# Kernel tuning notes

Measured on AMD Instinct MI355X. Metric: run time of the kernel, lower is better.

The kernel has to match this reference:

```python
import jax, jax.numpy as jnp
import numpy as np

EPS = 1e-8
EPS12 = 1e-12
TAU = 0.2
IOU_THRESHOLD = 0.5
NEG_INF = -1e9

N, C = 8192, 1024
HID, FGD, CLSD = 256, 64, 128


def setup_inputs() -> dict:
    key = jax.random.key(0)
    ks = jax.random.split(key, 16)
    roi_feats = jax.random.normal(ks[0], (N, C), dtype=jnp.float32)
    # labels in {-1 (ignore), 0 (bg), 1..20 (classes)}
    labels = jax.random.randint(ks[1], (N,), 0, 21, dtype=jnp.int64) - 1
    ious = jax.random.uniform(ks[2], (N,), dtype=jnp.float32)
    s = 0.02
    w1f = jax.random.normal(ks[3], (HID, C), dtype=jnp.float32) * s
    b1f = jnp.zeros((HID,), dtype=jnp.float32)
    w2f = jax.random.normal(ks[4], (FGD, HID), dtype=jnp.float32) * s
    b2f = jnp.zeros((FGD,), dtype=jnp.float32)
    w1c = jax.random.normal(ks[5], (HID, C), dtype=jnp.float32) * s
    b1c = jnp.zeros((HID,), dtype=jnp.float32)
    w2c = jax.random.normal(ks[6], (CLSD, HID), dtype=jnp.float32) * s
    b2c = jnp.zeros((CLSD,), dtype=jnp.float32)
    return {"roi_feats": roi_feats, "labels": labels, "ious": ious,
            "w1f": w1f, "b1f": b1f, "w2f": w2f, "b2f": b2f,
            "w1c": w1c, "b1c": b1c, "w2c": w2c, "b2c": b2c}


def _project_normalize(x, w1, b1, w2, b2):
    h = jax.nn.relu(x @ w1.T + b1)
    z = h @ w2.T + b2
    nrm = jnp.linalg.norm(z, axis=1, keepdims=True)  # F.normalize: z / max(||z||, eps)
    return z / jnp.maximum(nrm, EPS)


def _fg_bg_loss(z_fg, fg_mask, ignore_mask, iou_weight):
    n = z_fg.shape[0]
    anchor = fg_mask & ~ignore_mask
    eye = jnp.eye(n, dtype=bool)
    # pos_mask[i,j] = fg_mask[j] & ~ignore[j], self excluded
    pos = (fg_mask & ~ignore_mask)[None, :] & ~eye  # [N,N]
    sim = (z_fg @ z_fg.T) / TAU
    sim_exp = jnp.exp(sim) * (~eye).astype(sim.dtype)
    denom = sim_exp.sum(axis=1)  # [N]
    numer = jnp.sum(jnp.exp(sim) * pos.astype(sim.dtype), axis=1)  # [N]
    n_pos = pos.sum(axis=1)
    loss_i = -jnp.log((numer + EPS) / (denom + EPS))
    valid = anchor & (n_pos > 0)
    w = iou_weight
    num = jnp.sum(jnp.where(valid, loss_i * w, 0.0))
    den = jnp.sum(jnp.where(valid, w, 0.0)) + EPS
    return num / den


def _class_supcon_loss(z_cls, labels, fg_mask, ignore_mask, iou_weight):
    n = z_cls.shape[0]
    anchor = fg_mask & ~ignore_mask
    eye = jnp.eye(n, dtype=bool)
    valid_den = ~eye & ~ignore_mask[None, :]  # [N,N]
    # pos[i,j]: same label, j not ignored, labels[j] != 0, j != i, j valid
    pos = (labels[None, :] == labels[:, None]) & ~ignore_mask[None, :] & (labels[None, :] != 0)
    pos = pos & ~eye & valid_den
    sim = (z_cls @ z_cls.T) / TAU
    logits = jnp.where(valid_den, sim, NEG_INF)
    denom_log = jax.nn.logsumexp(logits, axis=1)  # [N]
    n_pos = pos.sum(axis=1)
    sum_pos = jnp.sum(jnp.where(pos, sim, 0.0), axis=1)
    n_pos_safe = jnp.maximum(n_pos, 1).astype(sim.dtype)
    loss_i = -(sum_pos - n_pos.astype(sim.dtype) * denom_log) / n_pos_safe
    valid = anchor & (n_pos > 0) & valid_den.any(axis=1)
    w = iou_weight
    num = jnp.sum(jnp.where(valid, loss_i * w, 0.0))
    den = jnp.sum(jnp.where(valid, w, 0.0)) + EPS12
    return num / den


def reference(roi_feats, labels, ious, w1f, b1f, w2f, b2f, w1c, b1c, w2c, b2c):
    z_fg = _project_normalize(roi_feats, w1f, b1f, w2f, b2f)
    z_cls = _project_normalize(roi_feats, w1c, b1c, w2c, b2c)
    ignore_mask = labels == -1
    bg_mask = (labels == 0) & ~ignore_mask
    fg_mask = (labels > 0) & ~ignore_mask
    iou_weight = jnp.where(ious > IOU_THRESHOLD, ious, 0.0)
    loss_fg_bg = _fg_bg_loss(z_fg, fg_mask, ignore_mask, iou_weight)
    loss_supcon = _class_supcon_loss(z_cls, labels, fg_mask, ignore_mask, iou_weight)
    # loss_weights = (1.0, 1.0); stacked as [loss_fg_bg, loss_supcon]
    return jnp.stack([loss_fg_bg * 1.0, loss_supcon * 1.0])
```

## Files before the change

### kernel.cpp

```cpp
#include <hip/hip_runtime.h>
#include <hip/hip_bf16.h>
#include <math.h>

#define N_ROI 8192
#define C_IN  1024
#define HIDD  256
#define FGD   64
#define CLSD  128
#define INV_TAU 5.0f
#define SCALE_LOG2E 7.2134752f
#define LN2F 0.69314718f

using frag_ab = __attribute__((ext_vector_type(8))) short;
using f32x16  = __attribute__((ext_vector_type(16))) float;

static __device__ __forceinline__ short f32_to_bf16_bits(float f) {
  unsigned u = __builtin_bit_cast(unsigned, f);
  u = (u + 0x7FFFu + ((u >> 16) & 1u)) >> 16;
  return (short)u;
}
static __device__ __forceinline__ float bf16_bits_to_f32(short b) {
  unsigned u = ((unsigned)(unsigned short)b) << 16;
  return __builtin_bit_cast(float, u);
}
static __device__ __forceinline__ float fast_exp2(float x) {
#if __has_builtin(__builtin_amdgcn_exp2f)
  return __builtin_amdgcn_exp2f(x);
#else
  return exp2f(x);
#endif
}
static __device__ __forceinline__ void async_copy16(const void* g, void* l) {
  __builtin_amdgcn_global_load_lds(
      (const __attribute__((address_space(1))) unsigned int*)g,
      (__attribute__((address_space(3))) unsigned int*)l, 16, 0, 0);
}

__global__ __launch_bounds__(256) void pack_zero_kernel(
    const float* __restrict__ X,
    const float* __restrict__ w1f, const float* __restrict__ w1c,
    const float* __restrict__ w2f, const float* __restrict__ w2c,
    short* __restrict__ W1pf, short* __restrict__ W1pc,
    short* __restrict__ W2pf, short* __restrict__ W2pc,
    short* __restrict__ Xp16,
    float* __restrict__ accum, int* __restrict__ cnt,
    float* __restrict__ Vc) {
  int b = blockIdx.x;
  if (b == 280) {
    int t = threadIdx.x;
    if (t < 8) accum[t] = 0.f;
    if (t < 24) cnt[t] = 0;
    for (int q = t; q < 2560; q += 256) Vc[q] = 0.f;
    return;
  }
  if (b >= 281) {
    int b2 = b - 281;
    int Mb = b2 >> 4, cpair = b2 & 15;
    int tid = threadIdx.x;
    int c = cpair * 2 + (tid >> 7);
    int tt = tid & 127;
    int lane = tt & 63, kh = tt >> 6;
    int row = lane & 31, hi = lane >> 5;
    const float* src = X + (size_t)(Mb * 32 + row) * C_IN + c * 32 + kh * 16 + hi * 8;
    float4 v0 = *(const float4*)src;
    float4 v1 = *(const float4*)(src + 4);
    union { short s[8]; uint4 v; } o;
    o.s[0] = f32_to_bf16_bits(v0.x); o.s[1] = f32_to_bf16_bits(v0.y);
    o.s[2] = f32_to_bf16_bits(v0.z); o.s[3] = f32_to_bf16_bits(v0.w);
    o.s[4] = f32_to_bf16_bits(v1.x); o.s[5] = f32_to_bf16_bits(v1.y);
    o.s[6] = f32_to_bf16_bits(v1.z); o.s[7] = f32_to_bf16_bits(v1.w);
    *(uint4*)&Xp16[((size_t)(Mb * 32 + c)) * 1024 + (size_t)tt * 8] = o.v;
    return;
  }
  const float* src; short* dst; int Ksh; int b0;
  if (b < 128)      { src = w1f; dst = W1pf; Ksh = 10; b0 = 0; }
  else if (b < 256) { src = w1c; dst = W1pc; Ksh = 10; b0 = 128; }
  else if (b < 264) { src = w2f; dst = W2pf; Ksh = 8;  b0 = 256; }
  else              { src = w2c; dst = W2pc; Ksh = 8;  b0 = 264; }
  int K = 1 << Ksh;
  int f = (b - b0) * 256 + threadIdx.x;
  int r = f >> (Ksh - 3);
  int c0 = (f & ((K >> 3) - 1)) << 3;
  float4 v0 = *(const float4*)(src + (size_t)r * K + c0);
  float4 v1 = *(const float4*)(src + (size_t)r * K + c0 + 4);
  union { short s[8]; uint4 v; } o;
  o.s[0] = f32_to_bf16_bits(v0.x); o.s[1] = f32_to_bf16_bits(v0.y);
  o.s[2] = f32_to_bf16_bits(v0.z); o.s[3] = f32_to_bf16_bits(v0.w);
  o.s[4] = f32_to_bf16_bits(v1.x); o.s[5] = f32_to_bf16_bits(v1.y);
  o.s[6] = f32_to_bf16_bits(v1.z); o.s[7] = f32_to_bf16_bits(v1.w);
  ((uint4*)dst)[(size_t)((r >> 5) * (K >> 4) + (c0 >> 4)) * 64 +
                ((c0 >> 3) & 1) * 32 + (r & 31)] = o.v;
}

template<int D>
__device__ __forceinline__ void gemm2_from_lds(
    const short* __restrict__ T2,
    const short* __restrict__ W2p, const float* __restrict__ b2,
    short* __restrict__ Zr, float* __restrict__ tii,
    short* __restrict__ T, int gt) {
  int lane = threadIdx.x & 63;
  const frag_ab* Wv = (const frag_ab*)W2p;
  constexpr int NT = D / 32;
  frag_ab a[16];
  #pragma unroll
  for (int kc = 0; kc < 16; ++kc)
    a[kc] = *(const frag_ab*)&T2[(lane & 31) * 264 + kc * 16 + (lane >> 5) * 8];
  f32x16 acc[NT];
  #pragma unroll
  for (int j = 0; j < NT; ++j)
    #pragma unroll
    for (int q = 0; q < 16; ++q) acc[j][q] = 0.f;
  #pragma unroll
  for (int kc = 0; kc < 16; ++kc)
    #pragma unroll
    for (int j = 0; j < NT; ++j)
      acc[j] = __builtin_amdgcn_mfma_f32_32x32x16_bf16(a[kc], Wv[(j * 16 + kc) * 64 + lane], acc[j], 0, 0, 0);
  int c = lane & 31, h = lane >> 5;
  float bb[NT];
  #pragma unroll
  for (int j = 0; j < NT; ++j) bb[j] = b2[j * 32 + c];
  float s1[16];
  #pragma unroll
  for (int r = 0; r < 16; ++r) {
    s1[r] = 0.f;
    #pragma unroll
    for (int j = 0; j < NT; ++j) {
      float v = acc[j][r] + bb[j];
      s1[r] += v * v;
    }
  }
  #pragma unroll
  for (int r = 0; r < 16; ++r)
    #pragma unroll
    for (int m = 1; m < 32; m <<= 1) s1[r] += __shfl_xor(s1[r], m);
  float s2[16];
  #pragma unroll
  for (int r = 0; r < 16; ++r) s2[r] = 0.f;
  #pragma unroll
  for (int j = 0; j < NT; ++j) {
    int cl = j * 32 + c;
    #pragma unroll
    for (int g = 0; g < 4; ++g) {
      short q0, q1, q2, q3;
      #pragma unroll
      for (int e = 0; e < 4; ++e) {
        int r = g * 4 + e;
        float sc = 1.f / fmaxf(sqrtf(s1[r]), 1e-8f);
        short qb = f32_to_bf16_bits((acc[j][r] + bb[j]) * sc);
        float zf = bf16_bits_to_f32(qb);
        s2[r] += zf * zf;
        if (e == 0) q0 = qb; else if (e == 1) q1 = qb; else if (e == 2) q2 = qb; else q3 = qb;
      }
      *(short4*)&T[cl * 36 + 4 * h + 8 * g] = make_short4(q0, q1, q2, q3);
    }
  }
  #pragma unroll
  for (int r = 0; r < 16; ++r)
    #pragma unroll
    for (int m = 1; m < 32; m <<= 1) s2[r] += __shfl_xor(s2[r], m);
  if (c == 0) {
    #pragma unroll
    for (int r = 0; r < 16; ++r)
      tii[gt * 32 + (r & 3) + 8 * (r >> 2) + 4 * h] = s2[r];
  }
  uint4* Zv = (uint4*)Zr;
  #pragma unroll
  for (int k = 0; k < D / 16; ++k) {
    int c0 = (2 * k + h) * 8;
    union { short s[8]; uint4 u; } o;
    #pragma unroll
    for (int e = 0; e < 8; ++e) o.s[e] = T[(c0 + e) * 36 + c];
    Zv[(size_t)(gt * (D / 16) + k) * 64 + h * 32 + c] = o.u;
  }
}

__global__ __launch_bounds__(256) void fused_mlp_kernel(
    const short* __restrict__ Xp16,
    const short* __restrict__ W1pf, const short* __restrict__ W1pc,
    const float* __restrict__ b1f, const float* __restrict__ b1c,
    const short* __restrict__ W2pf, const short* __restrict__ W2pc,
    const float* __restrict__ b2f, const float* __restrict__ b2c,
    short* __restrict__ Zrf, short* __restrict__ Zrc,
    float* __restrict__ tiif, float* __restrict__ tiic,
    const int* __restrict__ labels,
    float* __restrict__ Sfg, float* __restrict__ Pfg,
    float* __restrict__ Scls,
    float* __restrict__ pfv, float* __restrict__ nimv,
    int* __restrict__ cnt) {
  __shared__ short ringA[4 * 1024];
  __shared__ short T2[32 * 264];
  __shared__ short Tw[128 * 36];
  int tid = threadIdx.x, lane = tid & 63, wv = tid >> 6;
  int Mb = blockIdx.x, head = blockIdx.y;

  if (head == 0 && tid < 32) {
    int i = Mb * 32 + tid;
    Sfg[i] = 0.f; Pfg[i] = 0.f; Scls[i] = 0.f;
    int l = labels[i];
    pfv[i]  = (l > 0)  ? 1.f : 0.f;
    nimv[i] = (l != -1) ? 1.f : 0.f;
    int b = l + 1; if (b < 0) b = 0; if (b > 21) b = 21;
    atomicAdd(&cnt[b], 1);
  }
  __builtin_amdgcn_sched_barrier(0);
  asm volatile("s_waitcnt vmcnt(0)" ::: "memory");
  __builtin_amdgcn_sched_barrier(0);

  const short* Wp = head ? W1pc : W1pf;
  const float* b1 = head ? b1c  : b1f;
  const uint4* Wv4 = (const uint4*)Wp;
  int t127 = tid & 127;

  frag_ab breg[3][4];
  f32x16 acc[2];
  #pragma unroll
  for (int nt = 0; nt < 2; ++nt)
    #pragma unroll
    for (int q = 0; q < 16; ++q) acc[nt][q] = 0.f;

  auto stageA = [&](int c, int slot) {
    const short* src = Xp16 + ((size_t)(Mb * 32 + c)) * 1024 + (size_t)t127 * 8;
    async_copy16(src, &ringA[slot * 1024 + t127 * 8]);
  };
  auto loadB = [&](int c, int s) {
    #pragma unroll
    for (int kci = 0; kci < 2; ++kci)
      #pragma unroll
      for (int nt = 0; nt < 2; ++nt)
        breg[s][kci * 2 + nt] =
            *(const frag_ab*)&Wv4[(size_t)((wv * 2 + nt) * 64 + c * 2 + kci) * 64 + lane];
  };
  auto domfma = [&](int slot, int bank) {
    frag_ab a0 = *(const frag_ab*)&ringA[slot * 1024 + (0 * 64 + lane) * 8];
    frag_ab a1 = *(const frag_ab*)&ringA[slot * 1024 + (1 * 64 + lane) * 8];
    #pragma unroll
    for (int nt = 0; nt < 2; ++nt)
      acc[nt] = __builtin_amdgcn_mfma_f32_32x32x16_bf16(a0, breg[bank][nt], acc[nt], 0, 0, 0);
    #pragma unroll
    for (int nt = 0; nt < 2; ++nt)
      acc[nt] = __builtin_amdgcn_mfma_f32_32x32x16_bf16(a1, breg[bank][2 + nt], acc[nt], 0, 0, 0);
  };

  stageA(0, 0); stageA(1, 1); loadB(0, 0); stageA(2, 2); loadB(1, 1);

  #pragma unroll
  for (int c = 0; c < 32; ++c) {
    if (c < 30)       asm volatile("s_waitcnt vmcnt(5)" ::: "memory");
    else if (c == 30) asm volatile("s_waitcnt vmcnt(4)" ::: "memory");
    else              asm volatile("s_waitcnt vmcnt(0)" ::: "memory");
    __builtin_amdgcn_s_barrier();
    __builtin_amdgcn_sched_barrier(0);
    if (c + 3 < 32) stageA(c + 3, (c + 3) & 3);
    if (c + 2 < 32) loadB(c + 2, (c + 2) % 3);
    domfma(c & 3, c % 3);
  }
  {
    int cl31 = lane & 31, h = lane >> 5;
    #pragma unroll
    for (int nt = 0; nt < 2; ++nt) {
      int gc = wv * 64 + nt * 32 + cl31;
      float bb = b1[gc];
      #pragma unroll
      for (int q = 0; q < 16; ++q) {
        int row = (q & 3) + 8 * (q >> 2) + 4 * h;
        float x = fmaxf(acc[nt][q] + bb, 0.f);
        T2[row * 264 + gc] = f32_to_bf16_bits(x);
      }
    }
  }
  __syncthreads();

  if (wv == 0) {
    if (head == 0)
      gemm2_from_lds<FGD>(T2, W2pf, b2f, Zrf, tiif, Tw, Mb);
    else
      gemm2_from_lds<CLSD>(T2, W2pc, b2c, Zrc, tiic, Tw, Mb);
  }
}

__global__ __launch_bounds__(128) void classsum_kernel(
    const short* __restrict__ Zrc, const int* __restrict__ labels,
    float* __restrict__ Vc) {
  __shared__ int lidx[512];
  __shared__ int lcnt;
  int c = blockIdx.x + 1;
  int d = threadIdx.x;
  int j0 = blockIdx.y * 512;
  if (d == 0) lcnt = 0;
  __syncthreads();
  #pragma unroll
  for (int u = 0; u < 4; ++u) {
    int row = j0 + u * 128 + d;
    if (labels[row] == c) {
      int k = atomicAdd(&lcnt, 1);
      lidx[k] = row;
    }
  }
  __syncthreads();
  int n = lcnt;
  int kc = d >> 4, h = (d >> 3) & 1, e = d & 7;
  float acc = 0.f;
  for (int k = 0; k < n; ++k) {
    int row = lidx[k];
    int jt = row >> 5, r = row & 31;
    acc += bf16_bits_to_f32(
        Zrc[((size_t)((jt * 8 + kc) * 64 + h * 32 + r)) * 8 + e]);
  }
  atomicAdd(&Vc[(c - 1) * 128 + d], acc);
}

template<int D, int MODE, int NJT>
__device__ __forceinline__ void loss_body(
    const short* __restrict__ Zr,
    const float* __restrict__ maskv,
    float* __restrict__ Sg, float* __restrict__ Pg,
    short* __restrict__ smem) {
  constexpr int KC = D / 16;
  constexpr int JP = 2;
  constexpr int NIT = NJT / JP;
  constexpr int BUFQ = JP * KC * 512;
  constexpr int LD = BUFQ / 4096;
  int tid = threadIdx.x, lane = tid & 63, wv = tid >> 6;
  int itile = (blockIdx.x >> 1) * 8 + wv;
  int jt0 = blockIdx.y * NJT;
  int jlane = lane & 31;
  const frag_ab* Zrv = (const frag_ab*)Zr;

  frag_ab a[KC];
  #pragma unroll
  for (int kc = 0; kc < KC; ++kc) {
    frag_ab t = Zrv[(itile * KC + kc) * 64 + lane];
    #pragma unroll
    for (int e = 0; e < 8; ++e)
      t[e] = f32_to_bf16_bits(bf16_bits_to_f32(t[e]) * SCALE_LOG2E);
    a[kc] = t;
  }
  __builtin_amdgcn_sched_barrier(0);
  asm volatile("s_waitcnt vmcnt(0)" ::: "memory");
  __builtin_amdgcn_sched_barrier(0);

  short* b0 = smem;
  short* b1 = smem + BUFQ;
  short* b2 = smem + 2 * BUFQ;
  float* maskf = (float*)(smem + 3 * BUFQ);

  async_copy16(maskv + jt0 * 32 + (size_t)(tid & 127) * 4,
               maskf + (wv & 1) * 256);

  auto STAGE = [&](short* dst, int it) {
    const short* src = Zr + (size_t)(jt0 + it * JP) * KC * 512;
    #pragma unroll
    for (int u = 0; u < LD; ++u)
      async_copy16(src + (size_t)(u * 512 + tid) * 8, dst + u * 4096 + wv * 512);
  };

  STAGE(b0, 0); STAGE(b1, 1);

  float Ssum[16] = {}, Psum[16] = {};

  #pragma unroll 1
  for (int t = 0; t < NIT; ++t) {
    if (t < NIT - 1) {
      if constexpr (LD == 1) asm volatile("s_waitcnt vmcnt(1)" ::: "memory");
      else                   asm volatile("s_waitcnt vmcnt(2)" ::: "memory");
    } else {
      asm volatile("s_waitcnt vmcnt(0)" ::: "memory");
    }
    __builtin_amdgcn_s_barrier();
    __builtin_amdgcn_sched_barrier(0);
    if (t + 2 < NIT) STAGE(b2, t + 2);

    float m0 = maskf[t * 64 + jlane];
    float m1 = maskf[t * 64 + 32 + jlane];
    f32x16 acc0, acc1;
    #pragma unroll
    for (int q = 0; q < 16; ++q) { acc0[q] = 0.f; acc1[q] = 0.f; }
    #pragma unroll
    for (int kc = 0; kc < KC; ++kc) {
      frag_ab bb0 = *(const frag_ab*)&b0[(kc * 64 + lane) * 8];
      frag_ab bb1 = *(const frag_ab*)&b0[((KC + kc) * 64 + lane) * 8];
      acc0 = __builtin_amdgcn_mfma_f32_32x32x16_bf16(a[kc], bb0, acc0, 0, 0, 0);
      acc1 = __builtin_amdgcn_mfma_f32_32x32x16_bf16(a[kc], bb1, acc1, 0, 0, 0);
    }
    #pragma unroll
    for (int rr = 0; rr < 16; ++rr) {
      float e0 = fast_exp2(acc0[rr]);
      float e1 = fast_exp2(acc1[rr]);
      if (MODE == 0) {
        Ssum[rr] += e0 + e1;
        Psum[rr] = fmaf(m0, e0, fmaf(m1, e1, Psum[rr]));
      } else {
        Ssum[rr] = fmaf(m1, e1, fmaf(m0, e0, Ssum[rr]));
      }
    }
    short* tmp = b0; b0 = b1; b1 = b2; b2 = tmp;
  }

  #pragma unroll
  for (int r = 0; r < 16; ++r) {
    float s = Ssum[r], p = Psum[r];
    #pragma unroll
    for (int m = 1; m < 32; m <<= 1) {
      s += __shfl_xor(s, m);
      if (MODE == 0) p += __shfl_xor(p, m);
    }
    if ((lane & 31) == 0) {
      int row = (r & 3) + 8 * (r >> 2) + 4 * (lane >> 5);
      atomicAdd(&Sg[itile * 32 + row], s);
      if (MODE == 0) atomicAdd(&Pg[itile * 32 + row], p);
    }
  }
}

__global__ __launch_bounds__(512, 2) void loss_kernel(
    const short* __restrict__ Zrf, const short* __restrict__ Zrc,
    const float* __restrict__ pfv, const float* __restrict__ nimv,
    float* __restrict__ Sfg, float* __restrict__ Pfg,
    float* __restrict__ Scls) {
  __shared__ short smem[3 * 8192 + 1024];
  if ((blockIdx.x & 1) == 0)
    loss_body<FGD, 0, 16>(Zrf, pfv, Sfg, Pfg, smem);
  else
    loss_body<CLSD, 1, 16>(Zrc, nimv, Scls, nullptr, smem);
}

__global__ __launch_bounds__(256) void finalize_kernel(
    const float* __restrict__ Sfg, const float* __restrict__ Pfg,
    const float* __restrict__ Scls,
    const short* __restrict__ Zrc, const float* __restrict__ Vc,
    const float* __restrict__ tiif, const float* __restrict__ tiic,
    const int* __restrict__ labels, const float* __restrict__ ious,
    int* __restrict__ cnt, float* __restrict__ accum, float* __restrict__ out) {
  int i = blockIdx.x * 256 + threadIdx.x;
  int l = labels[i];
  float iv = ious[i];
  float w = (iv > 0.5f) ? iv : 0.f;
  int cntP = 0;
  #pragma unroll
  for (int b = 2; b <= 21; ++b) cntP += cnt[b];
  int cntNI = N_ROI - cnt[0];
  bool Pi = (l > 0);
  float numF = 0.f, denF = 0.f, numC = 0.f, denC = 0.f;
  float eF = __expf(INV_TAU * tiif[i]);
  float Sf = Sfg[i] - eF;
  float Pf = Pfg[i] - (Pi ? eF : 0.f);
  int nposF = cntP - (Pi ? 1 : 0);
  if (Pi && nposF > 0) {
    float lossF = logf((Sf + 1e-8f) / (Pf + 1e-8f));
    numF = lossF * w; denF = w;
  }
  float tC = INV_TAU * tiic[i];
  float eC = __expf(tC);
  float Sc = Scls[i] - ((l != -1) ? eC : 0.f);
  float SPdot = 0.f;
  if (Pi) {
    const float* V = Vc + (size_t)(l - 1) * 128;
    int jt = i >> 5, r = i & 31;
    #pragma unroll
    for (int kc = 0; kc < 8; ++kc)
      #pragma unroll
      for (int h = 0; h < 2; ++h) {
        frag_ab z = *(const frag_ab*)&Zrc[((size_t)((jt * 8 + kc) * 64 + h * 32 + r)) * 8];
        #pragma unroll
        for (int e = 0; e < 8; ++e)
          SPdot += bf16_bits_to_f32(z[e]) * V[kc * 16 + h * 8 + e];
      }
  }
  float SP = SPdot * INV_TAU - (Pi ? tC : 0.f);
  int nposC = Pi ? (cnt[l + 1] - 1) : 0;
  bool anyv = (cntNI - ((l != -1) ? 1 : 0)) > 0;
  if (Pi && nposC > 0 && anyv) {
    float lse = logf(Sc);
    float lossC = -(SP - (float)nposC * lse) / fmaxf((float)nposC, 1.f);
    numC = lossC * w; denC = w;
  }
  float v0 = numF, v1 = denF, v2 = numC, v3 = denC;
  #pragma unroll
  for (int m = 1; m < 64; m <<= 1) {
    v0 += __shfl_xor(v0, m); v1 += __shfl_xor(v1, m);
    v2 += __shfl_xor(v2, m); v3 += __shfl_xor(v3, m);
  }
  __shared__ float red[4][4];
  int lane = threadIdx.x & 63, wid = threadIdx.x >> 6;
  if (lane == 0) { red[wid][0]=v0; red[wid][1]=v1; red[wid][2]=v2; red[wid][3]=v3; }
  __syncthreads();
  if (threadIdx.x == 0) {
    float s0=0,s1=0,s2=0,s3=0;
    for (int q = 0; q < 4; ++q) { s0+=red[q][0]; s1+=red[q][1]; s2+=red[q][2]; s3+=red[q][3]; }
    atomicAdd(&accum[0], s0); atomicAdd(&accum[1], s1);
    atomicAdd(&accum[2], s2); atomicAdd(&accum[3], s3);
    __threadfence();
    int t = atomicAdd(&cnt[22], 1);
    if (t == 31) {
      __threadfence();
      out[0] = accum[0] / (accum[1] + 1e-8f);
      out[1] = accum[2] / (accum[3] + 1e-12f);
    }
  }
}

extern "C" void kernel_launch(void* const* d_in, const int* in_sizes, int n_in,
                              void* d_out, int out_size, void* d_ws, size_t ws_size,
                              hipStream_t stream) {
  const float* X    = (const float*)d_in[0];
  const int*  labels= (const int*)d_in[1];
  const float* ious = (const float*)d_in[2];
  const float* w1f  = (const float*)d_in[3];
  const float* b1f  = (const float*)d_in[4];
  const float* w2f  = (const float*)d_in[5];
  const float* b2f  = (const float*)d_in[6];
  const float* w1c  = (const float*)d_in[7];
  const float* b1c  = (const float*)d_in[8];
  const float* w2c  = (const float*)d_in[9];
  const float* b2c  = (const float*)d_in[10];
  float* out = (float*)d_out;

  char* w = (char*)d_ws;
  short* W1pf = (short*)w;            w += 524288;
  short* W1pc = (short*)w;            w += 524288;
  short* W2pf = (short*)w;            w += 32768;
  short* W2pc = (short*)w;            w += 65536;
  short* Zrf  = (short*)w;            w += 1048576;
  short* Zrc  = (short*)w;            w += 2097152;
  float* Sfg  = (float*)w;            w += 32768;
  float* Pfg  = (float*)w;            w += 32768;
  float* Scls = (float*)w;            w += 32768;
  float* SPc  = (float*)w;            w += 32768;
  float* tiif = (float*)w;            w += 32768;
  float* tiic = (float*)w;            w += 32768;
  float* pfv  = (float*)w;            w += 32768;
  float* nimv = (float*)w;            w += 32768;
  float* ljmv = (float*)w;            w += 32768;
  float* accum= (float*)w;            w += 32;
  int*   cnt  = (int*)w;              w += 96;
  float* Vc   = (float*)w;            w += 10240;
  short* Xp16 = (short*)w;            w += 16777216;
  (void)SPc; (void)ljmv;

  pack_zero_kernel<<<281 + 4096, 256, 0, stream>>>(X, w1f, w1c, w2f, w2c,
                                            W1pf, W1pc, W2pf, W2pc, Xp16,
                                            accum, cnt, Vc);

  fused_mlp_kernel<<<dim3(256, 2), 256, 0, stream>>>(Xp16, W1pf, W1pc, b1f, b1c,
                                            W2pf, W2pc, b2f, b2c,
                                            Zrf, Zrc, tiif, tiic,
                                            labels, Sfg, Pfg, Scls,
                                            pfv, nimv, cnt);

  classsum_kernel<<<dim3(20, 16), 128, 0, stream>>>(Zrc, labels, Vc);

  loss_kernel<<<dim3(64, 16), 512, 0, stream>>>(Zrf, Zrc, pfv, nimv,
                                                Sfg, Pfg, Scls);

  finalize_kernel<<<N_ROI/256, 256, 0, stream>>>(Sfg, Pfg, Scls, Zrc, Vc,
                                                 tiif, tiic,
                                                 labels, ious, cnt, accum, out);
}
```

Before: 189.0 us.

## Fuse X bf16 conversion into MLP kernel and merge classsum into loss launch

Removes the separate pass that converted the fp32 ROI features to a packed bf16 buffer. The MLP kernel now async-copies fp32 rows into a swizzled LDS ring and converts to bf16 just before each MFMA. This avoids writing and rereading the 16 MB intermediate, but doubles LDS staging traffic per K-chunk and adds conversion work to the inner loop. The class-sum kernel also becomes extra blocks of the loss kernel, saving one launch.

```diff
diff --git a/kernel.cpp b/kernel.cpp
--- a/kernel.cpp
+++ b/kernel.cpp
@@ -37,12 +37,10 @@
 }
 
 __global__ __launch_bounds__(256) void pack_zero_kernel(
-    const float* __restrict__ X,
     const float* __restrict__ w1f, const float* __restrict__ w1c,
     const float* __restrict__ w2f, const float* __restrict__ w2c,
     short* __restrict__ W1pf, short* __restrict__ W1pc,
     short* __restrict__ W2pf, short* __restrict__ W2pc,
-    short* __restrict__ Xp16,
     float* __restrict__ accum, int* __restrict__ cnt,
     float* __restrict__ Vc) {
   int b = blockIdx.x;
@@ -51,25 +49,6 @@
     if (t < 8) accum[t] = 0.f;
     if (t < 24) cnt[t] = 0;
     for (int q = t; q < 2560; q += 256) Vc[q] = 0.f;
-    return;
-  }
-  if (b >= 281) {
-    int b2 = b - 281;
-    int Mb = b2 >> 4, cpair = b2 & 15;
-    int tid = threadIdx.x;
-    int c = cpair * 2 + (tid >> 7);
-    int tt = tid & 127;
-    int lane = tt & 63, kh = tt >> 6;
-    int row = lane & 31, hi = lane >> 5;
-    const float* src = X + (size_t)(Mb * 32 + row) * C_IN + c * 32 + kh * 16 + hi * 8;
-    float4 v0 = *(const float4*)src;
-    float4 v1 = *(const float4*)(src + 4);
-    union { short s[8]; uint4 v; } o;
-    o.s[0] = f32_to_bf16_bits(v0.x); o.s[1] = f32_to_bf16_bits(v0.y);
-    o.s[2] = f32_to_bf16_bits(v0.z); o.s[3] = f32_to_bf16_bits(v0.w);
-    o.s[4] = f32_to_bf16_bits(v1.x); o.s[5] = f32_to_bf16_bits(v1.y);
-    o.s[6] = f32_to_bf16_bits(v1.z); o.s[7] = f32_to_bf16_bits(v1.w);
-    *(uint4*)&Xp16[((size_t)(Mb * 32 + c)) * 1024 + (size_t)tt * 8] = o.v;
     return;
   }
   const float* src; short* dst; int Ksh; int b0;
@@ -175,7 +154,7 @@
 }
 
 __global__ __launch_bounds__(256) void fused_mlp_kernel(
-    const short* __restrict__ Xp16,
+    const float* __restrict__ X,
     const short* __restrict__ W1pf, const short* __restrict__ W1pc,
     const float* __restrict__ b1f, const float* __restrict__ b1c,
     const short* __restrict__ W2pf, const short* __restrict__ W2pc,
@@ -187,7 +166,7 @@
     float* __restrict__ Scls,
     float* __restrict__ pfv, float* __restrict__ nimv,
     int* __restrict__ cnt) {
-  __shared__ short ringA[4 * 1024];
+  __shared__ float ringA[4 * 1024];
   __shared__ short T2[32 * 264];
   __shared__ short Tw[128 * 36];
   int tid = threadIdx.x, lane = tid & 63, wv = tid >> 6;
@@ -209,7 +188,17 @@
   const short* Wp = head ? W1pc : W1pf;
   const float* b1 = head ? b1c  : b1f;
   const uint4* Wv4 = (const uint4*)Wp;
-  int t127 = tid & 127;
+
+  int srow = wv * 8 + (lane >> 3);
+  int scol = ((lane & 7) ^ (lane >> 3)) * 4;
+  const float* Xrow = X + (size_t)(Mb * 32 + srow) * C_IN + scol;
+
+  int row = lane & 31, hi = lane >> 5;
+  int xm = (row & 7) << 4;
+  int o00 = ((row * 128 + (hi * 8) * 4) ^ xm) >> 2;
+  int o01 = ((row * 128 + (hi * 8 + 4) * 4) ^ xm) >> 2;
+  int o10 = ((row * 128 + (16 + hi * 8) * 4) ^ xm) >> 2;
+  int o11 = ((row * 128 + (16 + hi * 8 + 4) * 4) ^ xm) >> 2;
 
   frag_ab breg[3][4];
   f32x16 acc[2];
@@ -219,8 +208,7 @@
     for (int q = 0; q < 16; ++q) acc[nt][q] = 0.f;
 
   auto stageA = [&](int c, int slot) {
-    const short* src = Xp16 + ((size_t)(Mb * 32 + c)) * 1024 + (size_t)t127 * 8;
-    async_copy16(src, &ringA[slot * 1024 + t127 * 8]);
+    async_copy16(Xrow + c * 32, &ringA[slot * 1024 + wv * 256]);
   };
   auto loadB = [&](int c, int s) {
     #pragma unroll
@@ -230,9 +218,22 @@
         breg[s][kci * 2 + nt] =
             *(const frag_ab*)&Wv4[(size_t)((wv * 2 + nt) * 64 + c * 2 + kci) * 64 + lane];
   };
+  auto cvt8 = [&](float4 f0, float4 f1) -> frag_ab {
+    union { short s[8]; frag_ab f; } o;
+    o.s[0] = f32_to_bf16_bits(f0.x); o.s[1] = f32_to_bf16_bits(f0.y);
+    o.s[2] = f32_to_bf16_bits(f0.z); o.s[3] = f32_to_bf16_bits(f0.w);
+    o.s[4] = f32_to_bf16_bits(f1.x); o.s[5] = f32_to_bf16_bits(f1.y);
+    o.s[6] = f32_to_bf16_bits(f1.z); o.s[7] = f32_to_bf16_bits(f1.w);
+    return o.f;
+  };
   auto domfma = [&](int slot, int bank) {
-    frag_ab a0 = *(const frag_ab*)&ringA[slot * 1024 + (0 * 64 + lane) * 8];
-    frag_ab a1 = *(const frag_ab*)&ringA[slot * 1024 + (1 * 64 + lane) * 8];
+    const float* S = &ringA[slot * 1024];
+    float4 f00 = *(const float4*)&S[o00];
+    float4 f01 = *(const float4*)&S[o01];
+    float4 f10 = *(const float4*)&S[o10];
+    float4 f11 = *(const float4*)&S[o11];
+    frag_ab a0 = cvt8(f00, f01);
+    frag_ab a1 = cvt8(f10, f11);
     #pragma unroll
     for (int nt = 0; nt < 2; ++nt)
       acc[nt] = __builtin_amdgcn_mfma_f32_32x32x16_bf16(a0, breg[bank][nt], acc[nt], 0, 0, 0);
@@ -262,9 +263,9 @@
       float bb = b1[gc];
       #pragma unroll
       for (int q = 0; q < 16; ++q) {
-        int row = (q & 3) + 8 * (q >> 2) + 4 * h;
+        int rw = (q & 3) + 8 * (q >> 2) + 4 * h;
         float x = fmaxf(acc[nt][q] + bb, 0.f);
-        T2[row * 264 + gc] = f32_to_bf16_bits(x);
+        T2[rw * 264 + gc] = f32_to_bf16_bits(x);
       }
     }
   }
@@ -278,31 +279,32 @@
   }
 }
 
-__global__ __launch_bounds__(128) void classsum_kernel(
+__device__ __forceinline__ void classsum_body(
     const short* __restrict__ Zrc, const int* __restrict__ labels,
-    float* __restrict__ Vc) {
-  __shared__ int lidx[512];
-  __shared__ int lcnt;
-  int c = blockIdx.x + 1;
-  int d = threadIdx.x;
+    float* __restrict__ Vc, int* __restrict__ sh) {
+  int tid = threadIdx.x;
+  int unit = tid >> 7, d = tid & 127;
+  int c = (blockIdx.x - 64) * 4 + unit + 1;
   int j0 = blockIdx.y * 512;
-  if (d == 0) lcnt = 0;
+  int* lidx = sh + unit * 512;
+  int* lcnt = sh + 2048 + unit;
+  if (d == 0) *lcnt = 0;
   __syncthreads();
   #pragma unroll
   for (int u = 0; u < 4; ++u) {
-    int row = j0 + u * 128 + d;
-    if (labels[row] == c) {
-      int k = atomicAdd(&lcnt, 1);
-      lidx[k] = row;
+    int rw = j0 + u * 128 + d;
+    if (labels[rw] == c) {
+      int k = atomicAdd(lcnt, 1);
+      lidx[k] = rw;
     }
   }
   __syncthreads();
-  int n = lcnt;
+  int n = *lcnt;
   int kc = d >> 4, h = (d >> 3) & 1, e = d & 7;
   float acc = 0.f;
   for (int k = 0; k < n; ++k) {
-    int row = lidx[k];
-    int jt = row >> 5, r = row & 31;
+    int rw = lidx[k];
+    int jt = rw >> 5, r = rw & 31;
     acc += bf16_bits_to_f32(
         Zrc[((size_t)((jt * 8 + kc) * 64 + h * 32 + r)) * 8 + e]);
   }
@@ -405,19 +407,24 @@
       if (MODE == 0) p += __shfl_xor(p, m);
     }
     if ((lane & 31) == 0) {
-      int row = (r & 3) + 8 * (r >> 2) + 4 * (lane >> 5);
-      atomicAdd(&Sg[itile * 32 + row], s);
-      if (MODE == 0) atomicAdd(&Pg[itile * 32 + row], p);
+      int rw = (r & 3) + 8 * (r >> 2) + 4 * (lane >> 5);
+      atomicAdd(&Sg[itile * 32 + rw], s);
+      if (MODE == 0) atomicAdd(&Pg[itile * 32 + rw], p);
     }
   }
 }
 
 __global__ __launch_bounds__(512, 2) void loss_kernel(
     const short* __restrict__ Zrf, const short* __restrict__ Zrc,
+    const int* __restrict__ labels,
     const float* __restrict__ pfv, const float* __restrict__ nimv,
     float* __restrict__ Sfg, float* __restrict__ Pfg,
-    float* __restrict__ Scls) {
+    float* __restrict__ Scls, float* __restrict__ Vc) {
   __shared__ short smem[3 * 8192 + 1024];
+  if (blockIdx.x >= 64) {
+    classsum_body(Zrc, labels, Vc, (int*)smem);
+    return;
+  }
   if ((blockIdx.x & 1) == 0)
     loss_body<FGD, 0, 16>(Zrf, pfv, Sfg, Pfg, smem);
   else
@@ -534,23 +541,20 @@
   float* accum= (float*)w;            w += 32;
   int*   cnt  = (int*)w;              w += 96;
   float* Vc   = (float*)w;            w += 10240;
-  short* Xp16 = (short*)w;            w += 16777216;
   (void)SPc; (void)ljmv;
 
-  pack_zero_kernel<<<281 + 4096, 256, 0, stream>>>(X, w1f, w1c, w2f, w2c,
-                                            W1pf, W1pc, W2pf, W2pc, Xp16,
+  pack_zero_kernel<<<281, 256, 0, stream>>>(w1f, w1c, w2f, w2c,
+                                            W1pf, W1pc, W2pf, W2pc,
                                             accum, cnt, Vc);
 
-  fused_mlp_kernel<<<dim3(256, 2), 256, 0, stream>>>(Xp16, W1pf, W1pc, b1f, b1c,
+  fused_mlp_kernel<<<dim3(256, 2), 256, 0, stream>>>(X, W1pf, W1pc, b1f, b1c,
                                             W2pf, W2pc, b2f, b2c,
                                             Zrf, Zrc, tiif, tiic,
                                             labels, Sfg, Pfg, Scls,
                                             pfv, nimv, cnt);
 
-  classsum_kernel<<<dim3(20, 16), 128, 0, stream>>>(Zrc, labels, Vc);
-
-  loss_kernel<<<dim3(64, 16), 512, 0, stream>>>(Zrf, Zrc, pfv, nimv,
-                                                Sfg, Pfg, Scls);
+  loss_kernel<<<dim3(69, 16), 512, 0, stream>>>(Zrf, Zrc, labels, pfv, nimv,
+                                                Sfg, Pfg, Scls, Vc);
 
   finalize_kernel<<<N_ROI/256, 256, 0, stream>>>(Sfg, Pfg, Scls, Zrc, Vc,
                                                  tiif, tiic,
```

Measured after the change: 188.3 us. No clear change (-0.3%).

## Exploit similarity-matrix symmetry in loss kernel and fold classsum into it

Applied to the files above, without the earlier changes.

The loss kernel now computes only upper-triangular 256x256 tile pairs of the N×N similarity matrix. Off-diagonal tiles feed both row sums and column sums, using the anchor-side mask for the column contributions, which roughly halves the MFMA and exp work. The class-sum kernel is merged into the same launch as extra blocks to save a launch. The scale multiply moves from the A operand into the exp argument so the product stays symmetric, at the cost of extra column atomics, more registers and a serial tile-index decode loop.

```diff
diff --git a/kernel.cpp b/kernel.cpp
--- a/kernel.cpp
+++ b/kernel.cpp
@@ -278,62 +278,68 @@
   }
 }
 
-__global__ __launch_bounds__(128) void classsum_kernel(
+__device__ __forceinline__ void classsum_body(
     const short* __restrict__ Zrc, const int* __restrict__ labels,
-    float* __restrict__ Vc) {
-  __shared__ int lidx[512];
-  __shared__ int lcnt;
-  int c = blockIdx.x + 1;
-  int d = threadIdx.x;
-  int j0 = blockIdx.y * 512;
-  if (d == 0) lcnt = 0;
+    float* __restrict__ Vc, int* __restrict__ sh, int cs) {
+  int tid = threadIdx.x;
+  int unit = tid >> 7, d = tid & 127;
+  int cblk = cs % 5, chunk = cs / 5;
+  int c = cblk * 4 + unit + 1;
+  int j0 = chunk * 512;
+  int* lidx = sh + unit * 512;
+  int* lcnt = sh + 2048 + unit;
+  if (d == 0) *lcnt = 0;
   __syncthreads();
   #pragma unroll
   for (int u = 0; u < 4; ++u) {
-    int row = j0 + u * 128 + d;
-    if (labels[row] == c) {
-      int k = atomicAdd(&lcnt, 1);
-      lidx[k] = row;
+    int rw = j0 + u * 128 + d;
+    if (labels[rw] == c) {
+      int k = atomicAdd(lcnt, 1);
+      lidx[k] = rw;
     }
   }
   __syncthreads();
-  int n = lcnt;
+  int n = *lcnt;
   int kc = d >> 4, h = (d >> 3) & 1, e = d & 7;
   float acc = 0.f;
   for (int k = 0; k < n; ++k) {
-    int row = lidx[k];
-    int jt = row >> 5, r = row & 31;
+    int rw = lidx[k];
+    int jt = rw >> 5, r = rw & 31;
     acc += bf16_bits_to_f32(
         Zrc[((size_t)((jt * 8 + kc) * 64 + h * 32 + r)) * 8 + e]);
   }
   atomicAdd(&Vc[(c - 1) * 128 + d], acc);
 }
 
-template<int D, int MODE, int NJT>
+template<int D, int MODE, bool COLS>
 __device__ __forceinline__ void loss_body(
     const short* __restrict__ Zr,
     const float* __restrict__ maskv,
     float* __restrict__ Sg, float* __restrict__ Pg,
-    short* __restrict__ smem) {
+    short* __restrict__ smem, int gi, int gj) {
   constexpr int KC = D / 16;
   constexpr int JP = 2;
-  constexpr int NIT = NJT / JP;
+  constexpr int NIT = 4;
   constexpr int BUFQ = JP * KC * 512;
   constexpr int LD = BUFQ / 4096;
   int tid = threadIdx.x, lane = tid & 63, wv = tid >> 6;
-  int itile = (blockIdx.x >> 1) * 8 + wv;
-  int jt0 = blockIdx.y * NJT;
+  int itile = gi * 8 + wv;
+  int jt0 = gj * 8;
   int jlane = lane & 31;
   const frag_ab* Zrv = (const frag_ab*)Zr;
 
   frag_ab a[KC];
   #pragma unroll
-  for (int kc = 0; kc < KC; ++kc) {
-    frag_ab t = Zrv[(itile * KC + kc) * 64 + lane];
-    #pragma unroll
-    for (int e = 0; e < 8; ++e)
-      t[e] = f32_to_bf16_bits(bf16_bits_to_f32(t[e]) * SCALE_LOG2E);
-    a[kc] = t;
+  for (int kc = 0; kc < KC; ++kc)
+    a[kc] = Zrv[(itile * KC + kc) * 64 + lane];
+
+  float im[16];
+  if (COLS) {
+    #pragma unroll
+    for (int r = 0; r < 16; ++r) {
+      int row = (r & 3) + 8 * (r >> 2) + 4 * (lane >> 5);
+      im[r] = maskv[itile * 32 + row];
+    }
   }
   __builtin_amdgcn_sched_barrier(0);
   asm volatile("s_waitcnt vmcnt(0)" ::: "memory");
@@ -344,11 +350,10 @@
   short* b2 = smem + 2 * BUFQ;
   float* maskf = (float*)(smem + 3 * BUFQ);
 
-  async_copy16(maskv + jt0 * 32 + (size_t)(tid & 127) * 4,
-               maskf + (wv & 1) * 256);
-
-  auto STAGE = [&](short* dst, int it) {
-    const short* src = Zr + (size_t)(jt0 + it * JP) * KC * 512;
+  async_copy16(maskv + (size_t)jt0 * 32 + (size_t)lane * 4, maskf);
+
+  auto STAGE = [&](short* dst, int t) {
+    const short* src = Zr + (size_t)(jt0 + t * JP) * KC * 512;
     #pragma unroll
     for (int u = 0; u < LD; ++u)
       async_copy16(src + (size_t)(u * 512 + tid) * 8, dst + u * 4096 + wv * 512);
@@ -356,9 +361,10 @@
 
   STAGE(b0, 0); STAGE(b1, 1);
 
-  float Ssum[16] = {}, Psum[16] = {};
-
-  #pragma unroll 1
+  float rowS[16] = {}, rowP[16] = {};
+  float cS[8] = {}, cP[8] = {};
+
+  #pragma unroll
   for (int t = 0; t < NIT; ++t) {
     if (t < NIT - 1) {
       if constexpr (LD == 1) asm volatile("s_waitcnt vmcnt(1)" ::: "memory");
@@ -384,44 +390,87 @@
     }
     #pragma unroll
     for (int rr = 0; rr < 16; ++rr) {
-      float e0 = fast_exp2(acc0[rr]);
-      float e1 = fast_exp2(acc1[rr]);
+      float e0 = fast_exp2(acc0[rr] * SCALE_LOG2E);
+      float e1 = fast_exp2(acc1[rr] * SCALE_LOG2E);
       if (MODE == 0) {
-        Ssum[rr] += e0 + e1;
-        Psum[rr] = fmaf(m0, e0, fmaf(m1, e1, Psum[rr]));
+        rowS[rr] += e0 + e1;
+        rowP[rr] = fmaf(m0, e0, fmaf(m1, e1, rowP[rr]));
       } else {
-        Ssum[rr] = fmaf(m1, e1, fmaf(m0, e0, Ssum[rr]));
+        rowS[rr] = fmaf(m1, e1, fmaf(m0, e0, rowS[rr]));
       }
+      if (COLS) {
+        if (MODE == 0) {
+          cS[2 * t]     += e0;
+          cS[2 * t + 1] += e1;
+          cP[2 * t]     = fmaf(im[rr], e0, cP[2 * t]);
+          cP[2 * t + 1] = fmaf(im[rr], e1, cP[2 * t + 1]);
+        } else {
+          cS[2 * t]     = fmaf(im[rr], e0, cS[2 * t]);
+          cS[2 * t + 1] = fmaf(im[rr], e1, cS[2 * t + 1]);
+        }
+      }
     }
     short* tmp = b0; b0 = b1; b1 = b2; b2 = tmp;
   }
 
   #pragma unroll
   for (int r = 0; r < 16; ++r) {
-    float s = Ssum[r], p = Psum[r];
+    float s = rowS[r], p = rowP[r];
     #pragma unroll
     for (int m = 1; m < 32; m <<= 1) {
       s += __shfl_xor(s, m);
       if (MODE == 0) p += __shfl_xor(p, m);
     }
     if ((lane & 31) == 0) {
-      int row = (r & 3) + 8 * (r >> 2) + 4 * (lane >> 5);
-      atomicAdd(&Sg[itile * 32 + row], s);
-      if (MODE == 0) atomicAdd(&Pg[itile * 32 + row], p);
+      int rw = (r & 3) + 8 * (r >> 2) + 4 * (lane >> 5);
+      atomicAdd(&Sg[itile * 32 + rw], s);
+      if (MODE == 0) atomicAdd(&Pg[itile * 32 + rw], p);
+    }
+  }
+  if (COLS) {
+    #pragma unroll
+    for (int u = 0; u < 8; ++u) {
+      float v = cS[u] + __shfl_xor(cS[u], 32);
+      float vp = 0.f;
+      if (MODE == 0) vp = cP[u] + __shfl_xor(cP[u], 32);
+      if (lane < 32) {
+        atomicAdd(&Sg[(jt0 + u) * 32 + jlane], v);
+        if (MODE == 0) atomicAdd(&Pg[(jt0 + u) * 32 + jlane], vp);
+      }
     }
   }
 }
 
 __global__ __launch_bounds__(512, 2) void loss_kernel(
     const short* __restrict__ Zrf, const short* __restrict__ Zrc,
+    const int* __restrict__ labels,
     const float* __restrict__ pfv, const float* __restrict__ nimv,
     float* __restrict__ Sfg, float* __restrict__ Pfg,
-    float* __restrict__ Scls) {
+    float* __restrict__ Scls, float* __restrict__ Vc) {
   __shared__ short smem[3 * 8192 + 1024];
-  if ((blockIdx.x & 1) == 0)
-    loss_body<FGD, 0, 16>(Zrf, pfv, Sfg, Pfg, smem);
-  else
-    loss_body<CLSD, 1, 16>(Zrc, nimv, Scls, nullptr, smem);
+  int bx = blockIdx.x;
+  if (bx < 80) {
+    classsum_body(Zrc, labels, Vc, (int*)smem, bx);
+    return;
+  }
+  int li = bx - 80;
+  int mode = li & 1;
+  int p = li >> 1;
+  int gi, gj;
+  if (p < 32) { gi = p; gj = p; }
+  else {
+    int q = p - 32;
+    gi = 0;
+    while (q >= 31 - gi) { q -= 31 - gi; ++gi; }
+    gj = gi + 1 + q;
+  }
+  if (mode == 0) {
+    if (gi == gj) loss_body<FGD, 0, false>(Zrf, pfv, Sfg, Pfg, smem, gi, gj);
+    else          loss_body<FGD, 0, true >(Zrf, pfv, Sfg, Pfg, smem, gi, gj);
+  } else {
+    if (gi == gj) loss_body<CLSD, 1, false>(Zrc, nimv, Scls, nullptr, smem, gi, gj);
+    else          loss_body<CLSD, 1, true >(Zrc, nimv, Scls, nullptr, smem, gi, gj);
+  }
 }
 
 __global__ __launch_bounds__(256) void finalize_kernel(
@@ -547,10 +596,8 @@
                                             labels, Sfg, Pfg, Scls,
                                             pfv, nimv, cnt);
 
-  classsum_kernel<<<dim3(20, 16), 128, 0, stream>>>(Zrc, labels, Vc);
-
-  loss_kernel<<<dim3(64, 16), 512, 0, stream>>>(Zrf, Zrc, pfv, nimv,
-                                                Sfg, Pfg, Scls);
+  loss_kernel<<<80 + 2 * 528, 512, 0, stream>>>(Zrf, Zrc, labels, pfv, nimv,
+                                                Sfg, Pfg, Scls, Vc);
 
   finalize_kernel<<<N_ROI/256, 256, 0, stream>>>(Sfg, Pfg, Scls, Zrc, Vc,
                                                  tiif, tiic,
```

New measurement: 213.2 us. 12.8% more time.

## Split second projection GEMM across all four waves and coalesce X packing reads

Applied to the files above, without the earlier changes.

The second-layer GEMM plus normalization used to run on wave 0 alone while the other three waves sat idle. Each wave now computes one 32-column tile and writes partial row norms to shared memory, and a barrier-synchronised reduction combines them. The Z write-out loop is also spread across the waves. Separately, the X-to-bf16 packing kernel now reads contiguous row segments and writes them at a permuted address, which should coalesce the global loads, at the cost of scattered stores and two extra block-wide barriers.

```diff
diff --git a/kernel.cpp b/kernel.cpp
--- a/kernel.cpp
+++ b/kernel.cpp
@@ -59,9 +59,9 @@
     int tid = threadIdx.x;
     int c = cpair * 2 + (tid >> 7);
     int tt = tid & 127;
-    int lane = tt & 63, kh = tt >> 6;
-    int row = lane & 31, hi = lane >> 5;
-    const float* src = X + (size_t)(Mb * 32 + row) * C_IN + c * 32 + kh * 16 + hi * 8;
+    int r = tt >> 2;
+    int g = tt & 3;
+    const float* src = X + (size_t)(Mb * 32 + r) * C_IN + c * 32 + g * 8;
     float4 v0 = *(const float4*)src;
     float4 v1 = *(const float4*)(src + 4);
     union { short s[8]; uint4 v; } o;
@@ -69,7 +69,7 @@
     o.s[2] = f32_to_bf16_bits(v0.z); o.s[3] = f32_to_bf16_bits(v0.w);
     o.s[4] = f32_to_bf16_bits(v1.x); o.s[5] = f32_to_bf16_bits(v1.y);
     o.s[6] = f32_to_bf16_bits(v1.z); o.s[7] = f32_to_bf16_bits(v1.w);
-    *(uint4*)&Xp16[((size_t)(Mb * 32 + c)) * 1024 + (size_t)tt * 8] = o.v;
+    *(uint4*)&Xp16[((size_t)(Mb * 32 + c)) * 1024 + g * 256 + r * 8] = o.v;
     return;
   }
   const float* src; short* dst; int Ksh; int b0;
@@ -93,79 +93,91 @@
 }
 
 template<int D>
-__device__ __forceinline__ void gemm2_from_lds(
+__device__ __forceinline__ void gemm2_par(
     const short* __restrict__ T2,
     const short* __restrict__ W2p, const float* __restrict__ b2,
     short* __restrict__ Zr, float* __restrict__ tii,
-    short* __restrict__ T, int gt) {
-  int lane = threadIdx.x & 63;
-  const frag_ab* Wv = (const frag_ab*)W2p;
+    short* __restrict__ T, float* __restrict__ sred, int gt) {
   constexpr int NT = D / 32;
+  int tid = threadIdx.x, lane = tid & 63, wv = tid >> 6;
+  int c = lane & 31, h = lane >> 5;
+  bool act = (wv < NT);
+
   frag_ab a[16];
-  #pragma unroll
-  for (int kc = 0; kc < 16; ++kc)
-    a[kc] = *(const frag_ab*)&T2[(lane & 31) * 264 + kc * 16 + (lane >> 5) * 8];
-  f32x16 acc[NT];
-  #pragma unroll
-  for (int j = 0; j < NT; ++j)
-    #pragma unroll
-    for (int q = 0; q < 16; ++q) acc[j][q] = 0.f;
-  #pragma unroll
-  for (int kc = 0; kc < 16; ++kc)
-    #pragma unroll
-    for (int j = 0; j < NT; ++j)
-      acc[j] = __builtin_amdgcn_mfma_f32_32x32x16_bf16(a[kc], Wv[(j * 16 + kc) * 64 + lane], acc[j], 0, 0, 0);
-  int c = lane & 31, h = lane >> 5;
-  float bb[NT];
-  #pragma unroll
-  for (int j = 0; j < NT; ++j) bb[j] = b2[j * 32 + c];
-  float s1[16];
+  f32x16 acc;
+  float bb = 0.f;
+  if (act) {
+    #pragma unroll
+    for (int kc = 0; kc < 16; ++kc)
+      a[kc] = *(const frag_ab*)&T2[c * 264 + kc * 16 + h * 8];
+    #pragma unroll
+    for (int q = 0; q < 16; ++q) acc[q] = 0.f;
+    const frag_ab* Wv = (const frag_ab*)W2p;
+    #pragma unroll
+    for (int kc = 0; kc < 16; ++kc)
+      acc = __builtin_amdgcn_mfma_f32_32x32x16_bf16(a[kc], Wv[(wv * 16 + kc) * 64 + lane], acc, 0, 0, 0);
+    bb = b2[wv * 32 + c];
+    float s1[16];
+    #pragma unroll
+    for (int r = 0; r < 16; ++r) { float v = acc[r] + bb; s1[r] = v * v; }
+    #pragma unroll
+    for (int r = 0; r < 16; ++r)
+      #pragma unroll
+      for (int m = 1; m < 32; m <<= 1) s1[r] += __shfl_xor(s1[r], m);
+    if (c == 0) {
+      #pragma unroll
+      for (int r = 0; r < 16; ++r) sred[(wv * 2 + h) * 16 + r] = s1[r];
+    }
+  }
+  __syncthreads();
+  float s1f[16];
   #pragma unroll
   for (int r = 0; r < 16; ++r) {
-    s1[r] = 0.f;
-    #pragma unroll
-    for (int j = 0; j < NT; ++j) {
-      float v = acc[j][r] + bb[j];
-      s1[r] += v * v;
-    }
-  }
-  #pragma unroll
-  for (int r = 0; r < 16; ++r)
-    #pragma unroll
-    for (int m = 1; m < 32; m <<= 1) s1[r] += __shfl_xor(s1[r], m);
-  float s2[16];
-  #pragma unroll
-  for (int r = 0; r < 16; ++r) s2[r] = 0.f;
-  #pragma unroll
-  for (int j = 0; j < NT; ++j) {
-    int cl = j * 32 + c;
+    float s = sred[h * 16 + r];
+    #pragma unroll
+    for (int j = 1; j < NT; ++j) s += sred[(j * 2 + h) * 16 + r];
+    s1f[r] = s;
+  }
+  if (act) {
+    float s2[16];
+    #pragma unroll
+    for (int r = 0; r < 16; ++r) s2[r] = 0.f;
+    int cl = wv * 32 + c;
     #pragma unroll
     for (int g = 0; g < 4; ++g) {
       short q0, q1, q2, q3;
       #pragma unroll
       for (int e = 0; e < 4; ++e) {
         int r = g * 4 + e;
-        float sc = 1.f / fmaxf(sqrtf(s1[r]), 1e-8f);
-        short qb = f32_to_bf16_bits((acc[j][r] + bb[j]) * sc);
+        float sc = 1.f / fmaxf(sqrtf(s1f[r]), 1e-8f);
+        short qb = f32_to_bf16_bits((acc[r] + bb) * sc);
         float zf = bf16_bits_to_f32(qb);
         s2[r] += zf * zf;
         if (e == 0) q0 = qb; else if (e == 1) q1 = qb; else if (e == 2) q2 = qb; else q3 = qb;
       }
       *(short4*)&T[cl * 36 + 4 * h + 8 * g] = make_short4(q0, q1, q2, q3);
     }
-  }
-  #pragma unroll
-  for (int r = 0; r < 16; ++r)
-    #pragma unroll
-    for (int m = 1; m < 32; m <<= 1) s2[r] += __shfl_xor(s2[r], m);
-  if (c == 0) {
     #pragma unroll
     for (int r = 0; r < 16; ++r)
-      tii[gt * 32 + (r & 3) + 8 * (r >> 2) + 4 * h] = s2[r];
+      #pragma unroll
+      for (int m = 1; m < 32; m <<= 1) s2[r] += __shfl_xor(s2[r], m);
+    if (c == 0) {
+      #pragma unroll
+      for (int r = 0; r < 16; ++r) sred[128 + (wv * 2 + h) * 16 + r] = s2[r];
+    }
+  }
+  __syncthreads();
+  if (wv == 0 && c == 0) {
+    #pragma unroll
+    for (int r = 0; r < 16; ++r) {
+      float s = sred[128 + h * 16 + r];
+      #pragma unroll
+      for (int j = 1; j < NT; ++j) s += sred[128 + (j * 2 + h) * 16 + r];
+      tii[gt * 32 + (r & 3) + 8 * (r >> 2) + 4 * h] = s;
+    }
   }
   uint4* Zv = (uint4*)Zr;
-  #pragma unroll
-  for (int k = 0; k < D / 16; ++k) {
+  for (int k = wv; k < D / 16; k += 4) {
     int c0 = (2 * k + h) * 8;
     union { short s[8]; uint4 u; } o;
     #pragma unroll
@@ -190,6 +202,7 @@
   __shared__ short ringA[4 * 1024];
   __shared__ short T2[32 * 264];
   __shared__ short Tw[128 * 36];
+  __shared__ float sred[256];
   int tid = threadIdx.x, lane = tid & 63, wv = tid >> 6;
   int Mb = blockIdx.x, head = blockIdx.y;
 
@@ -270,12 +283,10 @@
   }
   __syncthreads();
 
-  if (wv == 0) {
-    if (head == 0)
-      gemm2_from_lds<FGD>(T2, W2pf, b2f, Zrf, tiif, Tw, Mb);
-    else
-      gemm2_from_lds<CLSD>(T2, W2pc, b2c, Zrc, tiic, Tw, Mb);
-  }
+  if (head == 0)
+    gemm2_par<FGD>(T2, W2pf, b2f, Zrf, tiif, Tw, sred, Mb);
+  else
+    gemm2_par<CLSD>(T2, W2pc, b2c, Zrc, tiic, Tw, sred, Mb);
 }
 
 __global__ __launch_bounds__(128) void classsum_kernel(
@@ -405,9 +416,9 @@
       if (MODE == 0) p += __shfl_xor(p, m);
     }
     if ((lane & 31) == 0) {
-      int row = (r & 3) + 8 * (r >> 2) + 4 * (lane >> 5);
-      atomicAdd(&Sg[itile * 32 + row], s);
-      if (MODE == 0) atomicAdd(&Pg[itile * 32 + row], p);
+      int rw = (r & 3) + 8 * (r >> 2) + 4 * (lane >> 5);
+      atomicAdd(&Sg[itile * 32 + rw], s);
+      if (MODE == 0) atomicAdd(&Pg[itile * 32 + rw], p);
     }
   }
 }
```

New measurement: 187.4 us. No clear change (-0.8%).
